# Kernel tuning notes

Measured on AMD Instinct MI355X. Metric: run time of the kernel, lower is better.

## Reference

```python
import jax, jax.numpy as jnp
import numpy as np

B, N, M = 8, 4096, 2048
IN_DIM, D, CTX_DIM = 512, 512, 768


def setup_inputs() -> dict:
    key = jax.random.key(0)
    k_h, k_hr, k_c, k_a, k_k, k_v, k_o = jax.random.split(key, 7)
    s = 0.02  # init scale for weights
    return {
        "h": jax.random.normal(k_h, (B, N, IN_DIM), dtype=jnp.float32),
        "h_retrieved": jax.random.normal(k_hr, (B, M, CTX_DIM), dtype=jnp.float32),
        # torch nn.Linear convention: weight is [out_features, in_features]
        "W_cond": jax.random.normal(k_c, (IN_DIM, CTX_DIM), dtype=jnp.float32) * s,
        "W_attn": jax.random.normal(k_a, (D, IN_DIM), dtype=jnp.float32) * s,
        "W_k": jax.random.normal(k_k, (D, IN_DIM), dtype=jnp.float32) * s,
        "W_v": jax.random.normal(k_v, (D, IN_DIM), dtype=jnp.float32) * s,
        "W_out": jax.random.normal(k_o, (IN_DIM, D), dtype=jnp.float32) * s,
    }


def reference(h, h_retrieved, W_cond, W_attn, W_k, W_v, W_out):
    # cond_flag is True since context_dim != in_dim
    hr = h_retrieved @ W_cond.T                      # [B, M, in_dim]
    attn = jax.nn.softmax(h @ W_attn.T, axis=-1)     # [B, N, d], softmax over channel dim
    kv_in = jnp.concatenate([h, hr], axis=1)         # [B, N+M, in_dim]
    k = kv_in @ W_k.T                                # [B, N+M, d]
    v = kv_in @ W_v.T                                # [B, N+M, d]
    f = jnp.einsum('bnd,bne->bde', k, v)             # K^T V: [B, d, d]
    h_aug = jnp.einsum('bnd,bde->bne', attn, f)      # [B, N, d]
    return h + h_aug @ W_out.T                       # [B, N, in_dim]
```

## Files before the change

kernel.cpp:

```cpp
#include <hip/hip_runtime.h>
#include <hip/hip_bf16.h>


typedef unsigned short u16;
typedef __bf16 bf16x8 __attribute__((ext_vector_type(8)));
typedef float  f32x4  __attribute__((ext_vector_type(4)));
typedef float  f32v4  __attribute__((ext_vector_type(4)));
typedef u16    u16v4  __attribute__((ext_vector_type(4)));
typedef u16    u16v8  __attribute__((ext_vector_type(8)));

__device__ __forceinline__ u16 f2bf(float f) {
  unsigned u = __builtin_bit_cast(unsigned, f);
  u = u + 0x7FFFu + ((u >> 16) & 1u);
  return (u16)(u >> 16);
}
__device__ __forceinline__ float bf2f(u16 s) {
  return __builtin_bit_cast(float, (unsigned)s << 16);
}

__global__ __launch_bounds__(256) void cvt_dual(const float* __restrict__ src,
                                                u16* __restrict__ dstN,
                                                u16* __restrict__ dstT,
                                                long src_bs, long dstT_bs) {
  __shared__ u16 tile[64][72];
  long bz = blockIdx.z;
  const float* S = src + bz * src_bs;
  u16* DN = dstN + bz * src_bs;
  u16* DT = dstT + bz * dstT_bs;
  int r0 = blockIdx.x * 64;
  int c0 = blockIdx.y * 64;
  int t  = threadIdx.x;
  int tr = t >> 2;
  int tc = (t & 3) * 16;
  const float* sp = &S[(long)(r0 + tr) * 512 + c0 + tc];
#pragma unroll
  for (int q = 0; q < 2; ++q) {
    f32v4 a = *(const f32v4*)(sp + q * 8);
    f32v4 b = *(const f32v4*)(sp + q * 8 + 4);
    u16v8 o;
    o[0] = f2bf(a[0]); o[1] = f2bf(a[1]); o[2] = f2bf(a[2]); o[3] = f2bf(a[3]);
    o[4] = f2bf(b[0]); o[5] = f2bf(b[1]); o[6] = f2bf(b[2]); o[7] = f2bf(b[3]);
    *(u16v8*)&DN[(long)(r0 + tr) * 512 + c0 + tc + q * 8] = o;
    *(u16v8*)&tile[tr][tc + q * 8] = o;
  }
  __syncthreads();
  int tr2 = t >> 3;
  int tc2 = (t & 7) * 8;
#pragma unroll
  for (int it = 0; it < 2; ++it) {
    int cr = it * 32 + tr2;
    u16v8 o;
#pragma unroll
    for (int j = 0; j < 8; ++j) o[j] = tile[tc2 + j][cr];
    *(u16v8*)&DT[(long)(c0 + cr) * 6144 + r0 + tc2] = o;
  }
}

__global__ __launch_bounds__(256) void prep_weights(
    const float* __restrict__ Wc, const float* __restrict__ Wa,
    const float* __restrict__ Wk, const float* __restrict__ Wv,
    const float* __restrict__ Wo,
    u16* __restrict__ wc, u16* __restrict__ wa, u16* __restrict__ wk,
    u16* __restrict__ wv, u16* __restrict__ wvT, u16* __restrict__ wo) {
  __shared__ u16 tile[64][72];
  int bx = blockIdx.x;
  int t = threadIdx.x;
  if (bx < 576) {
    const float* src; u16* dst; long base;
    if (bx < 192)      { src = Wc; dst = wc; base = (long)bx * 2048; }
    else if (bx < 320) { src = Wa; dst = wa; base = (long)(bx - 192) * 2048; }
    else if (bx < 448) { src = Wk; dst = wk; base = (long)(bx - 320) * 2048; }
    else               { src = Wo; dst = wo; base = (long)(bx - 448) * 2048; }
    long i = base + (long)t * 8;
    f32v4 a = *(const f32v4*)(src + i);
    f32v4 b = *(const f32v4*)(src + i + 4);
    u16v8 o;
    o[0] = f2bf(a[0]); o[1] = f2bf(a[1]); o[2] = f2bf(a[2]); o[3] = f2bf(a[3]);
    o[4] = f2bf(b[0]); o[5] = f2bf(b[1]); o[6] = f2bf(b[2]); o[7] = f2bf(b[3]);
    *(u16v8*)(dst + i) = o;
  } else {
    int b2 = bx - 576;
    int r0 = (b2 >> 3) * 64, c0 = (b2 & 7) * 64;
    int tr = t >> 2, tc = (t & 3) * 16;
    const float* sp = &Wv[(long)(r0 + tr) * 512 + c0 + tc];
#pragma unroll
    for (int q = 0; q < 2; ++q) {
      f32v4 a = *(const f32v4*)(sp + q * 8);
      f32v4 b = *(const f32v4*)(sp + q * 8 + 4);
      u16v8 o;
      o[0] = f2bf(a[0]); o[1] = f2bf(a[1]); o[2] = f2bf(a[2]); o[3] = f2bf(a[3]);
      o[4] = f2bf(b[0]); o[5] = f2bf(b[1]); o[6] = f2bf(b[2]); o[7] = f2bf(b[3]);
      *(u16v8*)&wv[(long)(r0 + tr) * 512 + c0 + tc + q * 8] = o;
      *(u16v8*)&tile[tr][tc + q * 8] = o;
    }
    __syncthreads();
    int tr2 = t >> 3, tc2 = (t & 7) * 8;
#pragma unroll
    for (int it = 0; it < 2; ++it) {
      int cr = it * 32 + tr2;
      u16v8 o;
#pragma unroll
      for (int j = 0; j < 8; ++j) o[j] = tile[tc2 + j][cr];
      *(u16v8*)&wvT[(long)(c0 + cr) * 512 + r0 + tc2] = o;
    }
  }
}

__global__ __launch_bounds__(256) void reduce8_bf16(const u16* __restrict__ parts,
                                                    u16* __restrict__ out) {
  long i = (((long)blockIdx.x * 256) + threadIdx.x) * 8;
  long b = i >> 18;
  long r = i & 262143;
  const u16* p = parts + b * 2097152 + r;
  float acc[8] = {};
#pragma unroll
  for (int s = 0; s < 8; ++s) {
    u16v8 v = *(const u16v8*)(p + (long)s * 262144);
#pragma unroll
    for (int j = 0; j < 8; ++j) acc[j] += bf2f(v[j]);
  }
  u16v8 o;
#pragma unroll
  for (int j = 0; j < 8; ++j) o[j] = f2bf(acc[j]);
  *(u16v8*)(out + i) = o;
}

template <int MODE>
__global__ __launch_bounds__(256) void gemm_nt(
    const u16* __restrict__ A, const u16* __restrict__ B, void* __restrict__ Cout,
    const float* __restrict__ Res, int K, int lda, int ldb, int ldc,
    long sA, long sB, long sC, long sS, long sRes, int kslices) {
  __shared__ __align__(16) char smem_c[65536];

  int gx = gridDim.x, gy = gridDim.y;
  int nwg = gx * gy * (int)gridDim.z;
  int flat = blockIdx.x + gx * (blockIdx.y + gy * blockIdx.z);
  if ((nwg & 7) == 0) { int q = nwg >> 3; flat = (flat & 7) * q + (flat >> 3); }
  int bx = flat % gx; int tmp = flat / gx; int by = tmp % gy; int z = tmp / gy;

  int b = z / kslices;
  int s = z - b * kslices;
  const u16* Ag = A + (long)b * sA + (long)s * K;
  const u16* Bg = B + (long)b * sB + (long)s * K;

  long m0 = (long)bx * 128;
  long n0 = (long)by * 128;

  int tid  = threadIdx.x;
  int lane = tid & 63;
  int wid  = tid >> 6;
  int wm = wid >> 1, wn = wid & 1;

  int srow = wid * 8 + (lane >> 3);
  int scol = (lane & 7) * 8;

  auto stageA = [&](u16* Asd, int k0) {
#pragma unroll
    for (int c = 0; c < 4; ++c) {
      int row = c * 32 + srow;
      __builtin_amdgcn_global_load_lds(
          (const __attribute__((address_space(1))) void*)(Ag + (m0 + row) * lda + k0 + scol),
          (__attribute__((address_space(3))) void*)(Asd + (c * 32 + wid * 8) * 64),
          16, 0, 0);
    }
  };
  auto stageB = [&](u16* Bsd, int k0) {
#pragma unroll
    for (int c = 0; c < 4; ++c) {
      int row = c * 32 + srow;
      __builtin_amdgcn_global_load_lds(
          (const __attribute__((address_space(1))) void*)(Bg + (n0 + row) * ldb + k0 + scol),
          (__attribute__((address_space(3))) void*)(Bsd + (c * 32 + wid * 8) * 64),
          16, 0, 0);
    }
  };

  f32x4 acc[4][4] = {};
  int nk = K >> 6;

  stageA((u16*)smem_c, 0);
  stageB((u16*)(smem_c + 32768), 0);

  for (int t = 0; t < nk; ++t) {
    u16* Asc = (u16*)(smem_c + (t & 1) * 16384);
    u16* Bsc = (u16*)(smem_c + 32768 + (t & 1) * 16384);
    if (t + 1 < nk) {
      u16* Asn = (u16*)(smem_c + ((t + 1) & 1) * 16384);
      u16* Bsn = (u16*)(smem_c + 32768 + ((t + 1) & 1) * 16384);
      stageA(Asn, (t + 1) * 64);
      stageB(Bsn, (t + 1) * 64);
      asm volatile("s_waitcnt vmcnt(8)\n\ts_barrier" ::: "memory");
    } else {
      asm volatile("s_waitcnt vmcnt(0)\n\ts_barrier" ::: "memory");
    }
#pragma unroll
    for (int kk = 0; kk < 2; ++kk) {
      int kofs = kk * 32 + (lane >> 4) * 8;
      bf16x8 af[4], bfr[4];
#pragma unroll
      for (int i = 0; i < 4; ++i) {
        af[i]  = *(const bf16x8*)&Asc[(wm * 64 + i * 16 + (lane & 15)) * 64 + kofs];
        bfr[i] = *(const bf16x8*)&Bsc[(wn * 64 + i * 16 + (lane & 15)) * 64 + kofs];
      }
#pragma unroll
      for (int i = 0; i < 4; ++i)
#pragma unroll
        for (int j = 0; j < 4; ++j)
          acc[i][j] = __builtin_amdgcn_mfma_f32_16x16x32_bf16(af[i], bfr[j], acc[i][j], 0, 0, 0);
    }
    asm volatile("s_barrier" ::: "memory");
  }

  float* ep = (float*)(smem_c + wid * 4608);
  long cb  = (long)b * sC + (long)s * sS;
  int row0 = (int)m0 + wm * 64;
  int colb = (int)n0 + wn * 64;
  int lq = lane >> 4;
  int lr = lane & 15;

#pragma unroll
  for (int i = 0; i < 4; ++i) {
#pragma unroll
    for (int j = 0; j < 4; ++j)
#pragma unroll
      for (int r = 0; r < 4; ++r)
        ep[(lq * 4 + r) * 72 + lr + j * 16] = acc[i][j][r];
#pragma unroll
    for (int p = 0; p < 4; ++p) {
      int rl = p * 4 + lq;
      f32x4 v = *(f32x4*)&ep[rl * 72 + lr * 4];
      long off = (long)(row0 + i * 16 + rl) * ldc + colb + lr * 4;
      if (MODE == 0) {
        u16v4 o;
#pragma unroll
        for (int t2 = 0; t2 < 4; ++t2) o[t2] = f2bf(v[t2]);
        *(u16v4*)((u16*)Cout + cb + off) = o;
      } else {
        const float* R = Res + (long)b * sRes;
        f32v4 rv = *(const f32v4*)&R[off];
        f32v4 ov;
#pragma unroll
        for (int t2 = 0; t2 < 4; ++t2) ov[t2] = v[t2] + rv[t2];
        *(f32v4*)((float*)Cout + cb + off) = ov;
      }
    }
  }
}

template <int MODE, bool AF32>
__global__ __launch_bounds__(256) void gemm64(
    const void* __restrict__ Ap, const u16* __restrict__ B, void* __restrict__ Cout,
    const float* __restrict__ Res, int K, int lda, int ldb, int ldc,
    long sA, long sB, long sC, long sRes) {
  __shared__ __align__(16) char smem_c[49152];

  int gx = gridDim.x, gy = gridDim.y;
  int nwg = gx * gy * (int)gridDim.z;
  int flat = blockIdx.x + gx * (blockIdx.y + gy * blockIdx.z);
  if ((nwg & 7) == 0) { int q = nwg >> 3; flat = (flat & 7) * q + (flat >> 3); }
  int bx = flat % gx; int tmp = flat / gx; int by = tmp % gy; int b = tmp / gy;

  long n0 = (long)bx * 128;
  long m0 = (long)by * 64;
  const u16* Ag = (const u16*)Ap + (long)b * sA;
  const float* Af = (const float*)Ap + (long)b * sA;
  const u16* Bg = B + (long)b * sB;

  int tid  = threadIdx.x;
  int lane = tid & 63;
  int wid  = tid >> 6;
  int wm = wid >> 1, wn = wid & 1;

  int srow = wid * 8 + (lane >> 3);
  int scol = (lane & 7) * 8;
  int arow = tid >> 2;
  int acol = (tid & 3) * 16;

  auto stageA = [&](u16* Asd, int k0) {
#pragma unroll
    for (int c = 0; c < 2; ++c) {
      int row = c * 32 + srow;
      __builtin_amdgcn_global_load_lds(
          (const __attribute__((address_space(1))) void*)(Ag + (m0 + row) * lda + k0 + scol),
          (__attribute__((address_space(3))) void*)(Asd + (c * 32 + wid * 8) * 64),
          16, 0, 0);
    }
  };
  auto stageB = [&](u16* Bsd, int k0) {
#pragma unroll
    for (int c = 0; c < 4; ++c) {
      int row = c * 32 + srow;
      __builtin_amdgcn_global_load_lds(
          (const __attribute__((address_space(1))) void*)(Bg + (n0 + row) * ldb + k0 + scol),
          (__attribute__((address_space(3))) void*)(Bsd + (c * 32 + wid * 8) * 64),
          16, 0, 0);
    }
  };
  auto cvtA = [&](u16* Asd, const f32v4& x0, const f32v4& x1,
                  const f32v4& x2, const f32v4& x3) {
    u16v8 o0, o1;
    o0[0] = f2bf(x0[0]); o0[1] = f2bf(x0[1]); o0[2] = f2bf(x0[2]); o0[3] = f2bf(x0[3]);
    o0[4] = f2bf(x1[0]); o0[5] = f2bf(x1[1]); o0[6] = f2bf(x1[2]); o0[7] = f2bf(x1[3]);
    o1[0] = f2bf(x2[0]); o1[1] = f2bf(x2[1]); o1[2] = f2bf(x2[2]); o1[3] = f2bf(x2[3]);
    o1[4] = f2bf(x3[0]); o1[5] = f2bf(x3[1]); o1[6] = f2bf(x3[2]); o1[7] = f2bf(x3[3]);
    *(u16v8*)&Asd[arow * 64 + acol] = o0;
    *(u16v8*)&Asd[arow * 64 + acol + 8] = o1;
  };

  f32x4 acc[2][4] = {};
  int nk = K >> 6;

  if constexpr (AF32) {
    const float* sp = Af + (m0 + arow) * (long)lda + acol;
    f32v4 x0 = *(const f32v4*)sp;
    f32v4 x1 = *(const f32v4*)(sp + 4);
    f32v4 x2 = *(const f32v4*)(sp + 8);
    f32v4 x3 = *(const f32v4*)(sp + 12);
    cvtA((u16*)smem_c, x0, x1, x2, x3);
    asm volatile("s_waitcnt lgkmcnt(0)" ::: "memory");
  } else {
    stageA((u16*)smem_c, 0);
  }
  stageB((u16*)(smem_c + 16384), 0);

  for (int t = 0; t < nk; ++t) {
    u16* Asc = (u16*)(smem_c + (t & 1) * 8192);
    u16* Bsc = (u16*)(smem_c + 16384 + (t & 1) * 16384);
    u16* Asn = (u16*)(smem_c + ((t + 1) & 1) * 8192);
    u16* Bsn = (u16*)(smem_c + 16384 + ((t + 1) & 1) * 16384);
    bool more = (t + 1) < nk;
    f32v4 x0, x1, x2, x3;
    if (more) {
      if constexpr (AF32) {
        const float* sp = Af + (m0 + arow) * (long)lda + (t + 1) * 64 + acol;
        x0 = *(const f32v4*)sp;
        x1 = *(const f32v4*)(sp + 4);
        x2 = *(const f32v4*)(sp + 8);
        x3 = *(const f32v4*)(sp + 12);
        stageB(Bsn, (t + 1) * 64);
        asm volatile("s_waitcnt vmcnt(8)\n\ts_barrier" ::: "memory");
      } else {
        stageA(Asn, (t + 1) * 64);
        stageB(Bsn, (t + 1) * 64);
        asm volatile("s_waitcnt vmcnt(6)\n\ts_barrier" ::: "memory");
      }
    } else {
      asm volatile("s_waitcnt vmcnt(0)\n\ts_barrier" ::: "memory");
    }
#pragma unroll
    for (int kk = 0; kk < 2; ++kk) {
      int kofs = kk * 32 + (lane >> 4) * 8;
      bf16x8 af[2], bfr[4];
#pragma unroll
      for (int i = 0; i < 2; ++i)
        af[i]  = *(const bf16x8*)&Asc[(wm * 32 + i * 16 + (lane & 15)) * 64 + kofs];
#pragma unroll
      for (int j = 0; j < 4; ++j)
        bfr[j] = *(const bf16x8*)&Bsc[(wn * 64 + j * 16 + (lane & 15)) * 64 + kofs];
#pragma unroll
      for (int i = 0; i < 2; ++i)
#pragma unroll
        for (int j = 0; j < 4; ++j)
          acc[i][j] = __builtin_amdgcn_mfma_f32_16x16x32_bf16(af[i], bfr[j], acc[i][j], 0, 0, 0);
    }
    if constexpr (AF32) {
      if (more) cvtA(Asn, x0, x1, x2, x3);
      asm volatile("s_waitcnt lgkmcnt(0)\n\ts_barrier" ::: "memory");
    } else {
      asm volatile("s_barrier" ::: "memory");
    }
  }

  int lq = lane >> 4;
  int lr = lane & 15;

  if (MODE == 0 || MODE == 1) {
    float* ep = (float*)(smem_c + wid * 4608);
    long cb  = (long)b * sC;
    int row0 = (int)m0 + wm * 32;
    int colb = (int)n0 + wn * 64;
#pragma unroll
    for (int i = 0; i < 2; ++i) {
#pragma unroll
      for (int j = 0; j < 4; ++j)
#pragma unroll
        for (int r = 0; r < 4; ++r)
          ep[(lq * 4 + r) * 72 + lr + j * 16] = acc[i][j][r];
#pragma unroll
      for (int p = 0; p < 4; ++p) {
        int rl = p * 4 + lq;
        f32x4 v = *(f32x4*)&ep[rl * 72 + lr * 4];
        long off = (long)(row0 + i * 16 + rl) * ldc + colb + lr * 4;
        if (MODE == 0) {
          u16v4 o;
#pragma unroll
          for (int t2 = 0; t2 < 4; ++t2) o[t2] = f2bf(v[t2]);
          *(u16v4*)((u16*)Cout + cb + off) = o;
        } else {
          const float* R = Res + (long)b * sRes;
          f32v4 rv = *(const f32v4*)&R[off];
          f32v4 ov;
#pragma unroll
          for (int t2 = 0; t2 < 4; ++t2) ov[t2] = v[t2] + rv[t2];
          *(f32v4*)((float*)Cout + cb + off) = ov;
        }
      }
    }
  } else {
    u16* tT = (u16*)smem_c;
#pragma unroll
    for (int i = 0; i < 2; ++i)
#pragma unroll
      for (int j = 0; j < 4; ++j)
#pragma unroll
        for (int r = 0; r < 4; ++r)
          tT[(wn * 64 + j * 16 + lr) * 72 + wm * 32 + i * 16 + lq * 4 + r] = f2bf(acc[i][j][r]);
    __syncthreads();
    long cb = (long)b * sC;
    int ct  = tid >> 1;
    int seg = (tid & 1) * 32;
    u16* dst = (u16*)Cout + cb + (long)(n0 + ct) * ldc + m0 + seg;
    const u16* srcl = &tT[ct * 72 + seg];
#pragma unroll
    for (int q = 0; q < 4; ++q)
      *(u16v8*)(dst + q * 8) = *(const u16v8*)(srcl + q * 8);
  }
}

__global__ __launch_bounds__(256, 2) void gemm_sm(
    const u16* __restrict__ A,
    const u16* __restrict__ Bw,
    u16* __restrict__ C) {
  __shared__ __align__(16) char smem[73728];
  u16* As = (u16*)smem;
  u16* Bs = (u16*)(smem + 8192);

  int nwg = gridDim.x;
  int flat = blockIdx.x;
  if ((nwg & 7) == 0) { int q = nwg >> 3; flat = (flat & 7) * q + (flat >> 3); }
  long m0 = (long)flat * 64;

  int tid = threadIdx.x;
  int lane = tid & 63;
  int wid = tid >> 6;

  int srow = wid * 8 + (lane >> 3);
  int scol = (lane & 7) * 8;

  f32x4 acc[4][8] = {};

  for (int k0 = 0; k0 < 512; k0 += 64) {
#pragma unroll
    for (int c = 0; c < 2; ++c) {
      int row = c * 32 + srow;
      __builtin_amdgcn_global_load_lds(
          (const __attribute__((address_space(1))) void*)(A + (m0 + row) * 512 + k0 + scol),
          (__attribute__((address_space(3))) void*)(As + (c * 32 + wid * 8) * 64),
          16, 0, 0);
    }
#pragma unroll
    for (int c = 0; c < 16; ++c) {
      int row = c * 32 + srow;
      __builtin_amdgcn_global_load_lds(
          (const __attribute__((address_space(1))) void*)(Bw + (long)row * 512 + k0 + scol),
          (__attribute__((address_space(3))) void*)(Bs + (c * 32 + wid * 8) * 64),
          16, 0, 0);
    }
    __syncthreads();
#pragma unroll
    for (int kk = 0; kk < 2; ++kk) {
      int kofs = kk * 32 + (lane >> 4) * 8;
      bf16x8 af[4], bfr[8];
#pragma unroll
      for (int i = 0; i < 4; ++i)
        af[i] = *(const bf16x8*)&As[(i * 16 + (lane & 15)) * 64 + kofs];
#pragma unroll
      for (int j = 0; j < 8; ++j)
        bfr[j] = *(const bf16x8*)&Bs[(wid * 128 + j * 16 + (lane & 15)) * 64 + kofs];
#pragma unroll
      for (int i = 0; i < 4; ++i)
#pragma unroll
        for (int j = 0; j < 8; ++j)
          acc[i][j] = __builtin_amdgcn_mfma_f32_16x16x32_bf16(af[i], bfr[j], acc[i][j], 0, 0, 0);
    }
    __syncthreads();
  }

  int lq = lane >> 4, lr = lane & 15;
  float* sm = (float*)smem;
  float* ss = (float*)(smem + 1024);

#pragma unroll
  for (int i = 0; i < 4; ++i)
#pragma unroll
    for (int r = 0; r < 4; ++r) {
      float m = acc[i][0][r];
#pragma unroll
      for (int j = 1; j < 8; ++j) m = fmaxf(m, acc[i][j][r]);
#pragma unroll
      for (int o = 1; o < 16; o <<= 1) m = fmaxf(m, __shfl_xor(m, o, 16));
      if (lr == 0) sm[(i * 16 + lq * 4 + r) * 4 + wid] = m;
    }
  __syncthreads();
  float rinv[4][4];
#pragma unroll
  for (int i = 0; i < 4; ++i)
#pragma unroll
    for (int r = 0; r < 4; ++r) {
      f32v4 g4 = *(const f32v4*)&sm[(i * 16 + lq * 4 + r) * 4];
      float gm = fmaxf(fmaxf(g4[0], g4[1]), fmaxf(g4[2], g4[3]));
      float s = 0.f;
#pragma unroll
      for (int j = 0; j < 8; ++j) {
        float e = __expf(acc[i][j][r] - gm);
        acc[i][j][r] = e;
        s += e;
      }
#pragma unroll
      for (int o = 1; o < 16; o <<= 1) s += __shfl_xor(s, o, 16);
      if (lr == 0) ss[(i * 16 + lq * 4 + r) * 4 + wid] = s;
    }
  __syncthreads();
#pragma unroll
  for (int i = 0; i < 4; ++i)
#pragma unroll
    for (int r = 0; r < 4; ++r) {
      f32v4 g4 = *(const f32v4*)&ss[(i * 16 + lq * 4 + r) * 4];
      rinv[i][r] = 1.0f / (g4[0] + g4[1] + g4[2] + g4[3]);
    }
  __syncthreads();

  float* ep = (float*)(smem + wid * 4608);
#pragma unroll
  for (int i = 0; i < 4; ++i) {
#pragma unroll
    for (int jh = 0; jh < 2; ++jh) {
#pragma unroll
      for (int j = 0; j < 4; ++j)
#pragma unroll
        for (int r = 0; r < 4; ++r)
          ep[(lq * 4 + r) * 72 + lr + j * 16] = acc[i][jh * 4 + j][r] * rinv[i][r];
#pragma unroll
      for (int p = 0; p < 4; ++p) {
        int rl = p * 4 + lq;
        f32x4 v = *(f32x4*)&ep[rl * 72 + lr * 4];
        u16v4 o;
#pragma unroll
        for (int t = 0; t < 4; ++t) o[t] = f2bf(v[t]);
        *(u16v4*)&C[(m0 + i * 16 + rl) * 512 + wid * 128 + jh * 64 + lr * 4] = o;
      }
    }
  }
}

extern "C" void kernel_launch(void* const* d_in, const int* in_sizes, int n_in,
                              void* d_out, int out_size, void* d_ws, size_t ws_size,
                              hipStream_t stream) {
  (void)in_sizes; (void)n_in; (void)out_size; (void)ws_size;
  const float* h    = (const float*)d_in[0];
  const float* hret = (const float*)d_in[1];
  const float* Wc   = (const float*)d_in[2];
  const float* Wa   = (const float*)d_in[3];
  const float* Wk   = (const float*)d_in[4];
  const float* Wv   = (const float*)d_in[5];
  const float* Wo   = (const float*)d_in[6];
  float* out = (float*)d_out;
  char*  ws  = (char*)d_ws;

  constexpr long MB = 1024 * 1024;
  u16*   w_cond = (u16*)(ws + 0);
  u16*   w_attn = (u16*)(ws + 786432);
  u16*   w_k    = (u16*)(ws + 1310720);
  u16*   w_v    = (u16*)(ws + 1835008);
  u16*   w_out  = (u16*)(ws + 2359296);
  u16*   w_vT   = (u16*)(ws + 2883584);
  u16*   h_bf   = (u16*)(ws + 4 * MB);
  u16*   gparts = (u16*)(ws + 4 * MB);
  u16*   attn   = (u16*)(ws + 36 * MB);
  u16*   g_bf   = (u16*)(ws + 68 * MB);
  u16*   u_mat  = (u16*)(ws + 72 * MB);
  u16*   v1     = (u16*)(ws + 73 * MB);
  u16*   f2t    = (u16*)(ws + 77 * MB);
  u16*   xt     = (u16*)(ws + 84 * MB);

  cvt_dual<<<dim3(64, 8, 8), 256, 0, stream>>>(h, h_bf, xt, 2097152L, 3145728L);
  prep_weights<<<640, 256, 0, stream>>>(Wc, Wa, Wk, Wv, Wo,
      w_cond, w_attn, w_k, w_v, w_vT, w_out);

  gemm64<3, true><<<dim3(4, 32, 8), 256, 0, stream>>>(hret, w_cond, xt + 4096, nullptr,
      768, 768, 768, 6144, 1572864L, 0, 3145728L, 0);

  gemm_sm<<<512, 256, 0, stream>>>(h_bf, w_attn, attn);

  gemm_nt<0><<<dim3(4, 4, 64), 256, 0, stream>>>(xt, xt, gparts, nullptr,
      768, 6144, 6144, 512, 3145728L, 3145728L, 2097152L, 262144L, 0, 8);
  reduce8_bf16<<<1024, 256, 0, stream>>>(gparts, g_bf);

  gemm64<0, false><<<dim3(4, 8, 1), 256, 0, stream>>>(w_out, w_vT, u_mat, nullptr,
      512, 512, 512, 512, 0, 0, 0, 0);
  gemm64<0, false><<<dim3(4, 8, 8), 256, 0, stream>>>(u_mat, g_bf, v1, nullptr,
      512, 512, 512, 512, 0, 262144L, 262144L, 0);
  gemm64<0, false><<<dim3(4, 8, 8), 256, 0, stream>>>(v1, w_k, f2t, nullptr,
      512, 512, 512, 512, 262144L, 0, 262144L, 0);

  gemm64<1, false><<<dim3(4, 64, 8), 256, 0, stream>>>(attn, f2t, out, h,
      512, 512, 512, 512, 2097152L, 262144L, 2097152L, 2097152L);
}
```

Measured before the change: 213.9 us.

## Exploit Gram symmetry, fuse h conversion into GEMM, use 128-tile GEMMs

The Gram GEMM (xt·xtᵀ) now computes only the upper-triangular 128x128 tiles (10 of 16) and writes each off-diagonal tile's transpose too, cutting MFMA work and operand traffic. The separate row-major bf16 copy of h is dropped: gemm_sm now loads fp32 h and converts to bf16 in registers while staging. The h_retrieved projection and the final output GEMM move from 64-row gemm64 tiles to the 128x128 gemm_nt kernel, which gains an fp32-A path for this. The trade-off is more register pressure and synchronous fp32 loads instead of async global-to-LDS copies for the A operand.

Result: no change. 210.3 us (-1.7%).

```diff
diff --git a/kernel.cpp b/kernel.cpp
--- a/kernel.cpp
+++ b/kernel.cpp
@@ -18,14 +18,12 @@
   return __builtin_bit_cast(float, (unsigned)s << 16);
 }
 
-__global__ __launch_bounds__(256) void cvt_dual(const float* __restrict__ src,
-                                                u16* __restrict__ dstN,
-                                                u16* __restrict__ dstT,
-                                                long src_bs, long dstT_bs) {
+__global__ __launch_bounds__(256) void cvt_T(const float* __restrict__ src,
+                                             u16* __restrict__ dstT,
+                                             long src_bs, long dstT_bs) {
   __shared__ u16 tile[64][72];
   long bz = blockIdx.z;
   const float* S = src + bz * src_bs;
-  u16* DN = dstN + bz * src_bs;
   u16* DT = dstT + bz * dstT_bs;
   int r0 = blockIdx.x * 64;
   int c0 = blockIdx.y * 64;
@@ -40,7 +38,6 @@
     u16v8 o;
     o[0] = f2bf(a[0]); o[1] = f2bf(a[1]); o[2] = f2bf(a[2]); o[3] = f2bf(a[3]);
     o[4] = f2bf(b[0]); o[5] = f2bf(b[1]); o[6] = f2bf(b[2]); o[7] = f2bf(b[3]);
-    *(u16v8*)&DN[(long)(r0 + tr) * 512 + c0 + tc + q * 8] = o;
     *(u16v8*)&tile[tr][tc + q * 8] = o;
   }
   __syncthreads();
@@ -125,9 +122,9 @@
   *(u16v8*)(out + i) = o;
 }
 
-template <int MODE>
+template <int MODE, bool AF32>
 __global__ __launch_bounds__(256) void gemm_nt(
-    const u16* __restrict__ A, const u16* __restrict__ B, void* __restrict__ Cout,
+    const void* __restrict__ Ap, const u16* __restrict__ B, void* __restrict__ Cout,
     const float* __restrict__ Res, int K, int lda, int ldb, int ldc,
     long sA, long sB, long sC, long sS, long sRes, int kslices) {
   __shared__ __align__(16) char smem_c[65536];
@@ -140,11 +137,20 @@
 
   int b = z / kslices;
   int s = z - b * kslices;
-  const u16* Ag = A + (long)b * sA + (long)s * K;
+
+  int mt = bx, nt = by;
+  if constexpr (MODE == 4) {
+    if (bx < 4)      { mt = 0; nt = bx; }
+    else if (bx < 7) { mt = 1; nt = bx - 3; }
+    else if (bx < 9) { mt = 2; nt = bx - 5; }
+    else             { mt = 3; nt = 3; }
+  }
+  long m0 = (long)mt * 128;
+  long n0 = (long)nt * 128;
+
+  const u16* Ag = (const u16*)Ap + (long)b * sA + (long)s * K;
+  const float* Af = (const float*)Ap + (long)b * sA;
   const u16* Bg = B + (long)b * sB + (long)s * K;
-
-  long m0 = (long)bx * 128;
-  long n0 = (long)by * 128;
 
   int tid  = threadIdx.x;
   int lane = tid & 63;
@@ -153,6 +159,8 @@
 
   int srow = wid * 8 + (lane >> 3);
   int scol = (lane & 7) * 8;
+  int arow  = tid >> 1;
+  int acolb = (tid & 1) * 32;
 
   auto stageA = [&](u16* Asd, int k0) {
 #pragma unroll
@@ -174,22 +182,52 @@
           16, 0, 0);
     }
   };
+  f32v4 xr[8];
+  auto loadA = [&](int k0) {
+    const float* sp = Af + (m0 + arow) * (long)lda + k0 + acolb;
+#pragma unroll
+    for (int q = 0; q < 8; ++q) xr[q] = *(const f32v4*)(sp + q * 4);
+  };
+  auto cvtA = [&](u16* Asd) {
+#pragma unroll
+    for (int q = 0; q < 4; ++q) {
+      u16v8 o;
+      o[0] = f2bf(xr[2*q][0]); o[1] = f2bf(xr[2*q][1]);
+      o[2] = f2bf(xr[2*q][2]); o[3] = f2bf(xr[2*q][3]);
+      o[4] = f2bf(xr[2*q+1][0]); o[5] = f2bf(xr[2*q+1][1]);
+      o[6] = f2bf(xr[2*q+1][2]); o[7] = f2bf(xr[2*q+1][3]);
+      *(u16v8*)&Asd[arow * 64 + acolb + q * 8] = o;
+    }
+  };
 
   f32x4 acc[4][4] = {};
   int nk = K >> 6;
 
-  stageA((u16*)smem_c, 0);
+  if constexpr (AF32) {
+    loadA(0);
+    cvtA((u16*)smem_c);
+    asm volatile("s_waitcnt lgkmcnt(0)" ::: "memory");
+  } else {
+    stageA((u16*)smem_c, 0);
+  }
   stageB((u16*)(smem_c + 32768), 0);
 
   for (int t = 0; t < nk; ++t) {
     u16* Asc = (u16*)(smem_c + (t & 1) * 16384);
     u16* Bsc = (u16*)(smem_c + 32768 + (t & 1) * 16384);
-    if (t + 1 < nk) {
-      u16* Asn = (u16*)(smem_c + ((t + 1) & 1) * 16384);
-      u16* Bsn = (u16*)(smem_c + 32768 + ((t + 1) & 1) * 16384);
-      stageA(Asn, (t + 1) * 64);
-      stageB(Bsn, (t + 1) * 64);
-      asm volatile("s_waitcnt vmcnt(8)\n\ts_barrier" ::: "memory");
+    u16* Asn = (u16*)(smem_c + ((t + 1) & 1) * 16384);
+    u16* Bsn = (u16*)(smem_c + 32768 + ((t + 1) & 1) * 16384);
+    bool more = (t + 1) < nk;
+    if (more) {
+      if constexpr (AF32) {
+        loadA((t + 1) * 64);
+        stageB(Bsn, (t + 1) * 64);
+        asm volatile("s_waitcnt vmcnt(12)\n\ts_barrier" ::: "memory");
+      } else {
+        stageA(Asn, (t + 1) * 64);
+        stageB(Bsn, (t + 1) * 64);
+        asm volatile("s_waitcnt vmcnt(8)\n\ts_barrier" ::: "memory");
+      }
     } else {
       asm volatile("s_waitcnt vmcnt(0)\n\ts_barrier" ::: "memory");
     }
@@ -208,50 +246,94 @@
         for (int j = 0; j < 4; ++j)
           acc[i][j] = __builtin_amdgcn_mfma_f32_16x16x32_bf16(af[i], bfr[j], acc[i][j], 0, 0, 0);
     }
-    asm volatile("s_barrier" ::: "memory");
-  }
-
-  float* ep = (float*)(smem_c + wid * 4608);
-  long cb  = (long)b * sC + (long)s * sS;
-  int row0 = (int)m0 + wm * 64;
-  int colb = (int)n0 + wn * 64;
+    if constexpr (AF32) {
+      if (more) cvtA(Asn);
+      asm volatile("s_waitcnt lgkmcnt(0)\n\ts_barrier" ::: "memory");
+    } else {
+      asm volatile("s_barrier" ::: "memory");
+    }
+  }
+
+  long cb = (long)b * sC + (long)s * sS;
   int lq = lane >> 4;
   int lr = lane & 15;
 
-#pragma unroll
-  for (int i = 0; i < 4; ++i) {
-#pragma unroll
-    for (int j = 0; j < 4; ++j)
-#pragma unroll
-      for (int r = 0; r < 4; ++r)
-        ep[(lq * 4 + r) * 72 + lr + j * 16] = acc[i][j][r];
-#pragma unroll
-    for (int p = 0; p < 4; ++p) {
-      int rl = p * 4 + lq;
-      f32x4 v = *(f32x4*)&ep[rl * 72 + lr * 4];
-      long off = (long)(row0 + i * 16 + rl) * ldc + colb + lr * 4;
-      if (MODE == 0) {
-        u16v4 o;
-#pragma unroll
-        for (int t2 = 0; t2 < 4; ++t2) o[t2] = f2bf(v[t2]);
-        *(u16v4*)((u16*)Cout + cb + off) = o;
-      } else {
-        const float* R = Res + (long)b * sRes;
-        f32v4 rv = *(const f32v4*)&R[off];
-        f32v4 ov;
-#pragma unroll
-        for (int t2 = 0; t2 < 4; ++t2) ov[t2] = v[t2] + rv[t2];
-        *(f32v4*)((float*)Cout + cb + off) = ov;
+  if constexpr (MODE == 0 || MODE == 1 || MODE == 4) {
+    float* ep = (float*)(smem_c + wid * 4608);
+    int row0 = (int)m0 + wm * 64;
+    int colb = (int)n0 + wn * 64;
+#pragma unroll
+    for (int i = 0; i < 4; ++i) {
+#pragma unroll
+      for (int j = 0; j < 4; ++j)
+#pragma unroll
+        for (int r = 0; r < 4; ++r)
+          ep[(lq * 4 + r) * 72 + lr + j * 16] = acc[i][j][r];
+#pragma unroll
+      for (int p = 0; p < 4; ++p) {
+        int rl = p * 4 + lq;
+        f32x4 v = *(f32x4*)&ep[rl * 72 + lr * 4];
+        long off = (long)(row0 + i * 16 + rl) * ldc + colb + lr * 4;
+        if (MODE == 0 || MODE == 4) {
+          u16v4 o;
+#pragma unroll
+          for (int t2 = 0; t2 < 4; ++t2) o[t2] = f2bf(v[t2]);
+          *(u16v4*)((u16*)Cout + cb + off) = o;
+        } else {
+          const float* R = Res + (long)b * sRes;
+          f32v4 rv = *(const f32v4*)&R[off];
+          f32v4 ov;
+#pragma unroll
+          for (int t2 = 0; t2 < 4; ++t2) ov[t2] = v[t2] + rv[t2];
+          *(f32v4*)((float*)Cout + cb + off) = ov;
+        }
       }
     }
-  }
-}
-
-template <int MODE, bool AF32>
+    if constexpr (MODE == 4) {
+      if (mt != nt) {
+        u16* tT = (u16*)(smem_c + 18432);
+#pragma unroll
+        for (int i = 0; i < 4; ++i)
+#pragma unroll
+          for (int j = 0; j < 4; ++j)
+#pragma unroll
+            for (int r = 0; r < 4; ++r)
+              tT[(wn * 64 + j * 16 + lr) * 136 + wm * 64 + i * 16 + lq * 4 + r] =
+                  f2bf(acc[i][j][r]);
+        __syncthreads();
+        int ct   = tid >> 1;
+        int half = (tid & 1) * 64;
+        u16* dst = (u16*)Cout + cb + (long)(n0 + ct) * ldc + m0 + half;
+        const u16* srcl = &tT[ct * 136 + half];
+#pragma unroll
+        for (int q = 0; q < 8; ++q)
+          *(u16v8*)(dst + q * 8) = *(const u16v8*)(srcl + q * 8);
+      }
+    }
+  } else {
+    u16* tT = (u16*)smem_c;
+#pragma unroll
+    for (int i = 0; i < 4; ++i)
+#pragma unroll
+      for (int j = 0; j < 4; ++j)
+#pragma unroll
+        for (int r = 0; r < 4; ++r)
+          tT[(wn * 64 + j * 16 + lr) * 136 + wm * 64 + i * 16 + lq * 4 + r] =
+              f2bf(acc[i][j][r]);
+    __syncthreads();
+    int ct   = tid >> 1;
+    int half = (tid & 1) * 64;
+    u16* dst = (u16*)Cout + cb + (long)(n0 + ct) * ldc + m0 + half;
+    const u16* srcl = &tT[ct * 136 + half];
+#pragma unroll
+    for (int q = 0; q < 8; ++q)
+      *(u16v8*)(dst + q * 8) = *(const u16v8*)(srcl + q * 8);
+  }
+}
+
 __global__ __launch_bounds__(256) void gemm64(
-    const void* __restrict__ Ap, const u16* __restrict__ B, void* __restrict__ Cout,
-    const float* __restrict__ Res, int K, int lda, int ldb, int ldc,
-    long sA, long sB, long sC, long sRes) {
+    const u16* __restrict__ A, const u16* __restrict__ B, u16* __restrict__ Cout,
+    int K, int lda, int ldb, int ldc, long sA, long sB, long sC) {
   __shared__ __align__(16) char smem_c[49152];
 
   int gx = gridDim.x, gy = gridDim.y;
@@ -262,8 +344,7 @@
 
   long n0 = (long)bx * 128;
   long m0 = (long)by * 64;
-  const u16* Ag = (const u16*)Ap + (long)b * sA;
-  const float* Af = (const float*)Ap + (long)b * sA;
+  const u16* Ag = A + (long)b * sA;
   const u16* Bg = B + (long)b * sB;
 
   int tid  = threadIdx.x;
@@ -273,8 +354,6 @@
 
   int srow = wid * 8 + (lane >> 3);
   int scol = (lane & 7) * 8;
-  int arow = tid >> 2;
-  int acol = (tid & 3) * 16;
 
   auto stageA = [&](u16* Asd, int k0) {
 #pragma unroll
@@ -296,31 +375,11 @@
           16, 0, 0);
     }
   };
-  auto cvtA = [&](u16* Asd, const f32v4& x0, const f32v4& x1,
-                  const f32v4& x2, const f32v4& x3) {
-    u16v8 o0, o1;
-    o0[0] = f2bf(x0[0]); o0[1] = f2bf(x0[1]); o0[2] = f2bf(x0[2]); o0[3] = f2bf(x0[3]);
-    o0[4] = f2bf(x1[0]); o0[5] = f2bf(x1[1]); o0[6] = f2bf(x1[2]); o0[7] = f2bf(x1[3]);
-    o1[0] = f2bf(x2[0]); o1[1] = f2bf(x2[1]); o1[2] = f2bf(x2[2]); o1[3] = f2bf(x2[3]);
-    o1[4] = f2bf(x3[0]); o1[5] = f2bf(x3[1]); o1[6] = f2bf(x3[2]); o1[7] = f2bf(x3[3]);
-    *(u16v8*)&Asd[arow * 64 + acol] = o0;
-    *(u16v8*)&Asd[arow * 64 + acol + 8] = o1;
-  };
 
   f32x4 acc[2][4] = {};
   int nk = K >> 6;
 
-  if constexpr (AF32) {
-    const float* sp = Af + (m0 + arow) * (long)lda + acol;
-    f32v4 x0 = *(const f32v4*)sp;
-    f32v4 x1 = *(const f32v4*)(sp + 4);
-    f32v4 x2 = *(const f32v4*)(sp + 8);
-    f32v4 x3 = *(const f32v4*)(sp + 12);
-    cvtA((u16*)smem_c, x0, x1, x2, x3);
-    asm volatile("s_waitcnt lgkmcnt(0)" ::: "memory");
-  } else {
-    stageA((u16*)smem_c, 0);
-  }
+  stageA((u16*)smem_c, 0);
   stageB((u16*)(smem_c + 16384), 0);
 
   for (int t = 0; t < nk; ++t) {
@@ -329,21 +388,10 @@
     u16* Asn = (u16*)(smem_c + ((t + 1) & 1) * 8192);
     u16* Bsn = (u16*)(smem_c + 16384 + ((t + 1) & 1) * 16384);
     bool more = (t + 1) < nk;
-    f32v4 x0, x1, x2, x3;
     if (more) {
-      if constexpr (AF32) {
-        const float* sp = Af + (m0 + arow) * (long)lda + (t + 1) * 64 + acol;
-        x0 = *(const f32v4*)sp;
-        x1 = *(const f32v4*)(sp + 4);
-        x2 = *(const f32v4*)(sp + 8);
-        x3 = *(const f32v4*)(sp + 12);
-        stageB(Bsn, (t + 1) * 64);
-        asm volatile("s_waitcnt vmcnt(8)\n\ts_barrier" ::: "memory");
-      } else {
-        stageA(Asn, (t + 1) * 64);
-        stageB(Bsn, (t + 1) * 64);
-        asm volatile("s_waitcnt vmcnt(6)\n\ts_barrier" ::: "memory");
-      }
+      stageA(Asn, (t + 1) * 64);
+      stageB(Bsn, (t + 1) * 64);
+      asm volatile("s_waitcnt vmcnt(6)\n\ts_barrier" ::: "memory");
     } else {
       asm volatile("s_waitcnt vmcnt(0)\n\ts_barrier" ::: "memory");
     }
@@ -363,72 +411,37 @@
         for (int j = 0; j < 4; ++j)
           acc[i][j] = __builtin_amdgcn_mfma_f32_16x16x32_bf16(af[i], bfr[j], acc[i][j], 0, 0, 0);
     }
-    if constexpr (AF32) {
-      if (more) cvtA(Asn, x0, x1, x2, x3);
-      asm volatile("s_waitcnt lgkmcnt(0)\n\ts_barrier" ::: "memory");
-    } else {
-      asm volatile("s_barrier" ::: "memory");
-    }
+    asm volatile("s_barrier" ::: "memory");
   }
 
   int lq = lane >> 4;
   int lr = lane & 15;
-
-  if (MODE == 0 || MODE == 1) {
-    float* ep = (float*)(smem_c + wid * 4608);
-    long cb  = (long)b * sC;
-    int row0 = (int)m0 + wm * 32;
-    int colb = (int)n0 + wn * 64;
-#pragma unroll
-    for (int i = 0; i < 2; ++i) {
-#pragma unroll
-      for (int j = 0; j < 4; ++j)
-#pragma unroll
-        for (int r = 0; r < 4; ++r)
-          ep[(lq * 4 + r) * 72 + lr + j * 16] = acc[i][j][r];
-#pragma unroll
-      for (int p = 0; p < 4; ++p) {
-        int rl = p * 4 + lq;
-        f32x4 v = *(f32x4*)&ep[rl * 72 + lr * 4];
-        long off = (long)(row0 + i * 16 + rl) * ldc + colb + lr * 4;
-        if (MODE == 0) {
-          u16v4 o;
-#pragma unroll
-          for (int t2 = 0; t2 < 4; ++t2) o[t2] = f2bf(v[t2]);
-          *(u16v4*)((u16*)Cout + cb + off) = o;
-        } else {
-          const float* R = Res + (long)b * sRes;
-          f32v4 rv = *(const f32v4*)&R[off];
-          f32v4 ov;
-#pragma unroll
-          for (int t2 = 0; t2 < 4; ++t2) ov[t2] = v[t2] + rv[t2];
-          *(f32v4*)((float*)Cout + cb + off) = ov;
-        }
-      }
-    }
-  } else {
-    u16* tT = (u16*)smem_c;
-#pragma unroll
-    for (int i = 0; i < 2; ++i)
-#pragma unroll
-      for (int j = 0; j < 4; ++j)
-#pragma unroll
-        for (int r = 0; r < 4; ++r)
-          tT[(wn * 64 + j * 16 + lr) * 72 + wm * 32 + i * 16 + lq * 4 + r] = f2bf(acc[i][j][r]);
-    __syncthreads();
-    long cb = (long)b * sC;
-    int ct  = tid >> 1;
-    int seg = (tid & 1) * 32;
-    u16* dst = (u16*)Cout + cb + (long)(n0 + ct) * ldc + m0 + seg;
-    const u16* srcl = &tT[ct * 72 + seg];
-#pragma unroll
-    for (int q = 0; q < 4; ++q)
-      *(u16v8*)(dst + q * 8) = *(const u16v8*)(srcl + q * 8);
+  float* ep = (float*)(smem_c + wid * 4608);
+  long cb  = (long)b * sC;
+  int row0 = (int)m0 + wm * 32;
+  int colb = (int)n0 + wn * 64;
+#pragma unroll
+  for (int i = 0; i < 2; ++i) {
+#pragma unroll
+    for (int j = 0; j < 4; ++j)
+#pragma unroll
+      for (int r = 0; r < 4; ++r)
+        ep[(lq * 4 + r) * 72 + lr + j * 16] = acc[i][j][r];
+#pragma unroll
+    for (int p = 0; p < 4; ++p) {
+      int rl = p * 4 + lq;
+      f32x4 v = *(f32x4*)&ep[rl * 72 + lr * 4];
+      long off = (long)(row0 + i * 16 + rl) * ldc + colb + lr * 4;
+      u16v4 o;
+#pragma unroll
+      for (int t2 = 0; t2 < 4; ++t2) o[t2] = f2bf(v[t2]);
+      *(u16v4*)(Cout + cb + off) = o;
+    }
   }
 }
 
 __global__ __launch_bounds__(256, 2) void gemm_sm(
-    const u16* __restrict__ A,
+    const float* __restrict__ A,
     const u16* __restrict__ Bw,
     u16* __restrict__ C) {
   __shared__ __align__(16) char smem[73728];
@@ -446,18 +459,17 @@
 
   int srow = wid * 8 + (lane >> 3);
   int scol = (lane & 7) * 8;
+  int arow  = tid >> 2;
+  int acolb = (tid & 3) * 16;
 
   f32x4 acc[4][8] = {};
 
   for (int k0 = 0; k0 < 512; k0 += 64) {
-#pragma unroll
-    for (int c = 0; c < 2; ++c) {
-      int row = c * 32 + srow;
-      __builtin_amdgcn_global_load_lds(
-          (const __attribute__((address_space(1))) void*)(A + (m0 + row) * 512 + k0 + scol),
-          (__attribute__((address_space(3))) void*)(As + (c * 32 + wid * 8) * 64),
-          16, 0, 0);
-    }
+    const float* sp = A + (m0 + arow) * 512 + k0 + acolb;
+    f32v4 x0 = *(const f32v4*)sp;
+    f32v4 x1 = *(const f32v4*)(sp + 4);
+    f32v4 x2 = *(const f32v4*)(sp + 8);
+    f32v4 x3 = *(const f32v4*)(sp + 12);
 #pragma unroll
     for (int c = 0; c < 16; ++c) {
       int row = c * 32 + srow;
@@ -466,6 +478,13 @@
           (__attribute__((address_space(3))) void*)(Bs + (c * 32 + wid * 8) * 64),
           16, 0, 0);
     }
+    u16v8 o0, o1;
+    o0[0] = f2bf(x0[0]); o0[1] = f2bf(x0[1]); o0[2] = f2bf(x0[2]); o0[3] = f2bf(x0[3]);
+    o0[4] = f2bf(x1[0]); o0[5] = f2bf(x1[1]); o0[6] = f2bf(x1[2]); o0[7] = f2bf(x1[3]);
+    o1[0] = f2bf(x2[0]); o1[1] = f2bf(x2[1]); o1[2] = f2bf(x2[2]); o1[3] = f2bf(x2[3]);
+    o1[4] = f2bf(x3[0]); o1[5] = f2bf(x3[1]); o1[6] = f2bf(x3[2]); o1[7] = f2bf(x3[3]);
+    *(u16v8*)&As[arow * 64 + acolb] = o0;
+    *(u16v8*)&As[arow * 64 + acolb + 8] = o1;
     __syncthreads();
 #pragma unroll
     for (int kk = 0; kk < 2; ++kk) {
@@ -574,7 +593,6 @@
   u16*   w_v    = (u16*)(ws + 1835008);
   u16*   w_out  = (u16*)(ws + 2359296);
   u16*   w_vT   = (u16*)(ws + 2883584);
-  u16*   h_bf   = (u16*)(ws + 4 * MB);
   u16*   gparts = (u16*)(ws + 4 * MB);
   u16*   attn   = (u16*)(ws + 36 * MB);
   u16*   g_bf   = (u16*)(ws + 68 * MB);
@@ -583,26 +601,26 @@
   u16*   f2t    = (u16*)(ws + 77 * MB);
   u16*   xt     = (u16*)(ws + 84 * MB);
 
-  cvt_dual<<<dim3(64, 8, 8), 256, 0, stream>>>(h, h_bf, xt, 2097152L, 3145728L);
+  cvt_T<<<dim3(64, 8, 8), 256, 0, stream>>>(h, xt, 2097152L, 3145728L);
   prep_weights<<<640, 256, 0, stream>>>(Wc, Wa, Wk, Wv, Wo,
       w_cond, w_attn, w_k, w_v, w_vT, w_out);
 
-  gemm64<3, true><<<dim3(4, 32, 8), 256, 0, stream>>>(hret, w_cond, xt + 4096, nullptr,
-      768, 768, 768, 6144, 1572864L, 0, 3145728L, 0);
-
-  gemm_sm<<<512, 256, 0, stream>>>(h_bf, w_attn, attn);
-
-  gemm_nt<0><<<dim3(4, 4, 64), 256, 0, stream>>>(xt, xt, gparts, nullptr,
+  gemm_nt<3, true><<<dim3(16, 4, 8), 256, 0, stream>>>(hret, w_cond, xt + 4096, nullptr,
+      768, 768, 768, 6144, 1572864L, 0, 3145728L, 0, 0, 1);
+
+  gemm_sm<<<512, 256, 0, stream>>>(h, w_attn, attn);
+
+  gemm_nt<4, false><<<dim3(10, 1, 64), 256, 0, stream>>>(xt, xt, gparts, nullptr,
       768, 6144, 6144, 512, 3145728L, 3145728L, 2097152L, 262144L, 0, 8);
   reduce8_bf16<<<1024, 256, 0, stream>>>(gparts, g_bf);
 
-  gemm64<0, false><<<dim3(4, 8, 1), 256, 0, stream>>>(w_out, w_vT, u_mat, nullptr,
-      512, 512, 512, 512, 0, 0, 0, 0);
-  gemm64<0, false><<<dim3(4, 8, 8), 256, 0, stream>>>(u_mat, g_bf, v1, nullptr,
-      512, 512, 512, 512, 0, 262144L, 262144L, 0);
-  gemm64<0, false><<<dim3(4, 8, 8), 256, 0, stream>>>(v1, w_k, f2t, nullptr,
-      512, 512, 512, 512, 262144L, 0, 262144L, 0);
-
-  gemm64<1, false><<<dim3(4, 64, 8), 256, 0, stream>>>(attn, f2t, out, h,
-      512, 512, 512, 512, 2097152L, 262144L, 2097152L, 2097152L);
-}
+  gemm64<<<dim3(4, 8, 1), 256, 0, stream>>>(w_out, w_vT, u_mat,
+      512, 512, 512, 512, 0, 0, 0);
+  gemm64<<<dim3(4, 8, 8), 256, 0, stream>>>(u_mat, g_bf, v1,
+      512, 512, 512, 512, 0, 262144L, 262144L);
+  gemm64<<<dim3(4, 8, 8), 256, 0, stream>>>(v1, w_k, f2t,
+      512, 512, 512, 512, 262144L, 0, 262144L);
+
+  gemm_nt<1, false><<<dim3(32, 4, 8), 256, 0, stream>>>(attn, f2t, out, h,
+      512, 512, 512, 512, 2097152L, 262144L, 2097152L, 0, 2097152L, 1);
+}
```
